# Optimization experiments

Hardware: AMD Instinct MI355X
Metric: run time of the kernel (lower is better)

The kernel has to match this reference:

```python
import jax, jax.numpy as jnp
import numpy as np

EMBED_DIM = 1024
NUM_HEADS = 16
HEAD_DIM = EMBED_DIM // NUM_HEADS
MAX_SEQ_LEN = 2048
ROPE_BASE = 10000.0


def _rope_tables(head_dim, max_seq_len, base):
    # inv_freq: (head_dim/2,)
    inv_freq = 1.0 / base ** (jnp.arange(0, head_dim, 2, dtype=jnp.float32) / head_dim)
    positions = jnp.arange(max_seq_len, dtype=jnp.float32)
    angles = positions[:, None] * inv_freq[None, :]  # (S, head_dim/2)
    # Original repeat_interleaves then slices [0::2], which recovers per-pair angles.
    return jnp.cos(angles), jnp.sin(angles)


def _apply_rope(x, cos, sin):
    # x: (B, H, S, D); cos/sin: (S, D/2)
    x_even = x[..., 0::2]
    x_odd = x[..., 1::2]
    c = cos[None, None, :, :]
    s = sin[None, None, :, :]
    x_even_rot = x_even * c - x_odd * s
    x_odd_rot = x_even * s + x_odd * c
    # interleave back: stack pairs on last dim and flatten
    x_rot = jnp.stack([x_even_rot, x_odd_rot], axis=-1)
    return x_rot.reshape(x.shape)


def setup_inputs() -> dict:
    key = jax.random.key(0)
    k1, k2, k3, k4 = jax.random.split(key, 4)
    B, S, E = 2, 2048, EMBED_DIM
    x = jax.random.normal(k1, (B, S, E), dtype=jnp.float32)
    bound_in = np.sqrt(6.0 / (3 * E + E)).astype(np.float32)
    in_proj_weight = jax.random.uniform(k2, (3 * E, E), minval=-bound_in, maxval=bound_in, dtype=jnp.float32)
    in_proj_bias = jnp.zeros((3 * E,), dtype=jnp.float32)
    bound_out = np.sqrt(6.0 / (E + E)).astype(np.float32)
    out_proj_weight = jax.random.uniform(k3, (E, E), minval=-bound_out, maxval=bound_out, dtype=jnp.float32)
    out_proj_bias = jnp.zeros((E,), dtype=jnp.float32)
    return {
        "query": x,
        "key": x,
        "value": x,
        "in_proj_weight": in_proj_weight,
        "in_proj_bias": in_proj_bias,
        "out_proj_weight": out_proj_weight,
        "out_proj_bias": out_proj_bias,
    }


def reference(query, key, value, in_proj_weight, in_proj_bias, out_proj_weight, out_proj_bias):
    B, S, E = query.shape
    H, D = NUM_HEADS, HEAD_DIM
    cos, sin = _rope_tables(D, MAX_SEQ_LEN, ROPE_BASE)
    cos, sin = cos[:S], sin[:S]

    # fused QKV projection (note: original applies in_proj to `query` only — self-attention)
    qkv = query @ in_proj_weight.T + in_proj_bias  # (B, S, 3E)
    q, k, v = jnp.split(qkv, 3, axis=-1)
    q = q.reshape(B, S, H, D).transpose(0, 2, 1, 3)  # (B, H, S, D)
    k = k.reshape(B, S, H, D).transpose(0, 2, 1, 3)
    v = v.reshape(B, S, H, D).transpose(0, 2, 1, 3)

    q = _apply_rope(q, cos, sin)
    k = _apply_rope(k, cos, sin)

    scale = 1.0 / np.sqrt(D).astype(np.float32)
    scores = jnp.einsum("bhqd,bhkd->bhqk", q, k) * scale
    attn = jax.nn.softmax(scores, axis=-1)
    out = jnp.einsum("bhqk,bhkd->bhqd", attn, v)  # (B, H, S, D)
    out = out.transpose(0, 2, 1, 3).reshape(B, S, E)
    return out @ out_proj_weight.T + out_proj_bias
```

## Files before the change

### kernel.cpp

```cpp
#include <hip/hip_runtime.h>
#include <hip/hip_bf16.h>
#include <cstdint>
#include <cstddef>

typedef __bf16 bf16;
typedef bf16 bf16x2 __attribute__((ext_vector_type(2)));
typedef bf16 bf16x4 __attribute__((ext_vector_type(4)));
typedef bf16 bf16x8 __attribute__((ext_vector_type(8)));
typedef float f32x4 __attribute__((ext_vector_type(4)));
typedef float f32x16 __attribute__((ext_vector_type(16)));

#define SEQ 2048
#define EMB 1024
#define NH 16
#define HD 64
#define BSZ 2
#define MROWS (BSZ*SEQ)

__device__ __forceinline__ void gload_lds16(const void* g, void* lds) {
  __builtin_amdgcn_global_load_lds((__attribute__((address_space(1))) void*)g,
                                   (__attribute__((address_space(3))) void*)lds,
                                   16, 0, 0);
}

__global__ void prep_kernel(const float* __restrict__ s0, bf16* __restrict__ d0, int n0_4,
                            const float* __restrict__ s1, bf16* __restrict__ d1, int n1_4,
                            const float* __restrict__ s2, bf16* __restrict__ d2, int n2_4,
                            float* __restrict__ cosT, float* __restrict__ sinT) {
  int j = blockIdx.x * blockDim.x + threadIdx.x;
  const float* s; bf16* d;
  if (j < n0_4) { s = s0; d = d0; }
  else {
    int j1 = j - n0_4;
    if (j1 < n1_4) { s = s1; d = d1; j = j1; }
    else {
      int j2 = j1 - n1_4;
      if (j2 < n2_4) { s = s2; d = d2; j = j2; }
      else {
        int idx = j2 - n2_4;
        if (idx >= SEQ * 32) return;
        int ss = idx >> 5, jj = idx & 31;
        float ex = (2.0f * (float)jj) / 64.0f;
        float inv = 1.0f / powf(10000.0f, ex);
        float ang = (float)ss * inv;
        cosT[idx] = cosf(ang);
        sinT[idx] = sinf(ang);
        return;
      }
    }
  }
  const float4 v = reinterpret_cast<const float4*>(s)[j];
  bf16x4 o;
  o[0] = (bf16)v.x; o[1] = (bf16)v.y; o[2] = (bf16)v.z; o[3] = (bf16)v.w;
  reinterpret_cast<bf16x4*>(d)[j] = o;
}

template<int EPI, int BM>
__launch_bounds__(256)
__global__ void gemm_bt(const bf16* __restrict__ A, const bf16* __restrict__ B,
                        const float* __restrict__ bias,
                        float* __restrict__ Cf,
                        bf16* __restrict__ qb, bf16* __restrict__ kb, bf16* __restrict__ vt,
                        const float* __restrict__ cosT, const float* __restrict__ sinT,
                        int Ndim, int Kdim) {
  constexpr int MREP = BM / 32;
  __shared__ __align__(16) bf16 Alds[2][BM * 32];
  __shared__ __align__(16) bf16 Blds[2][128 * 32];
  const int tid = threadIdx.x;
  const int wave = tid >> 6, lane = tid & 63;
  const int wr = wave >> 1, wc = wave & 1;
  const int bm = blockIdx.x * BM, bn = blockIdx.y * 128;

  f32x4 acc[MREP][4] = {};

  const int srow = lane >> 2;
  const int scol = (((lane & 3) ^ ((lane >> 3) & 3)) * 8);
  const int rchunk = (((lane >> 4) ^ ((lane >> 1) & 3)) * 8);

  for (int kt = 0; kt < Kdim; kt += 64) {
#pragma unroll
    for (int hf = 0; hf < 2; hf++) {
      char* aldsb = (char*)Alds[hf];
      char* bldsb = (char*)Blds[hf];
      const int kc = kt + hf * 32;
#pragma unroll
      for (int c = 0; c < BM / 64; c++)
        gload_lds16(A + (size_t)(bm + (wave + 4 * c) * 16 + srow) * Kdim + kc + scol,
                    aldsb + wave * 1024 + c * 4096);
      gload_lds16(B + (size_t)(bn + wave * 16 + srow) * Kdim + kc + scol, bldsb + wave * 1024);
      gload_lds16(B + (size_t)(bn + (wave + 4) * 16 + srow) * Kdim + kc + scol, bldsb + wave * 1024 + 4096);
    }
    __syncthreads();
#pragma unroll
    for (int hf = 0; hf < 2; hf++) {
      bf16x8 af[MREP], bfr[4];
#pragma unroll
      for (int m = 0; m < MREP; m++)
        af[m] = *reinterpret_cast<const bf16x8*>(Alds[hf] + (wr * (BM / 2) + m * 16 + (lane & 15)) * 32 + rchunk);
#pragma unroll
      for (int n = 0; n < 4; n++)
        bfr[n] = *reinterpret_cast<const bf16x8*>(Blds[hf] + (wc * 64 + n * 16 + (lane & 15)) * 32 + rchunk);
#pragma unroll
      for (int m = 0; m < MREP; m++)
#pragma unroll
        for (int n = 0; n < 4; n++)
          acc[m][n] = __builtin_amdgcn_mfma_f32_16x16x32_bf16(af[m], bfr[n], acc[m][n], 0, 0, 0);
    }
    __syncthreads();
  }

  if (EPI == 1 && bn >= 2 * EMB) {
#pragma unroll
    for (int m = 0; m < MREP; m++) {
#pragma unroll
      for (int n = 0; n < 4; n++) {
        const int col = bn + wc * 64 + n * 16 + (lane & 15);
        const int rem = col & 1023;
        const int h = rem >> 6, d = rem & 63;
        const int row0 = bm + wr * (BM / 2) + m * 16 + (lane >> 4) * 4;
        const int b = row0 >> 11, s0 = row0 & (SEQ - 1);
        const int g = (s0 >> 2) & 3;
        const int s0p = (s0 & ~15) | ((((g & 1) << 1) | (g >> 1)) << 2);
        const float bs = bias[col];
        bf16x4 o;
#pragma unroll
        for (int r = 0; r < 4; r++) o[r] = (bf16)(acc[m][n][r] + bs);
        *reinterpret_cast<bf16x4*>(vt + (((size_t)(b * NH + h) * HD) + d) * SEQ + s0p) = o;
      }
    }
  } else {
#pragma unroll
    for (int m = 0; m < MREP; m++) {
#pragma unroll
      for (int n = 0; n < 4; n++) {
#pragma unroll
        for (int r = 0; r < 4; r++) {
          const int row = bm + wr * (BM / 2) + m * 16 + (lane >> 4) * 4 + r;
          const int col = bn + wc * 64 + n * 16 + (lane & 15);
          const float v = acc[m][n][r] + bias[col];
          if (EPI == 0) {
            Cf[(size_t)row * Ndim + col] = v;
          } else {
            const int b = row >> 11, s = row & (SEQ - 1);
            const int which = col >> 10, rem = col & 1023;
            const int h = rem >> 6, d = rem & 63;
            const float vp = __shfl_xor(v, 1, 64);
            const int jj = d >> 1;
            const float c = cosT[(s << 5) + jj], sn = sinT[(s << 5) + jj];
            float vr = (d & 1) ? (vp * sn + v * c) : (v * c - vp * sn);
            if (which == 0) {
              vr *= 0.18033688f;
              qb[(((size_t)(b * NH + h) * SEQ) + s) * HD + d] = (bf16)vr;
            } else {
              kb[(((size_t)(b * NH + h) * SEQ) + s) * HD + d] = (bf16)vr;
            }
          }
        }
      }
    }
  }
}

__device__ __forceinline__ unsigned pk2(float a, float b) {
  bf16x2 t; t[0] = (bf16)a; t[1] = (bf16)b;
  unsigned u; __builtin_memcpy(&u, &t, 4); return u;
}

#if __has_builtin(__builtin_amdgcn_exp2f)
#define FEXP2(x) __builtin_amdgcn_exp2f(x)
#else
#define FEXP2(x) exp2f(x)
#endif

#define SSHIFT (-17.3123405f)

#define KPITCH 144

#define STAGE_LOAD(KV0) do { \
  kr0 = *(const int4*)(Kb + (size_t)((KV0) + (gtid >> 3)) * HD + (gtid & 7) * 8); \
  kr1 = *(const int4*)(Kb + (size_t)((KV0) + 32 + (gtid >> 3)) * HD + (gtid & 7) * 8); \
  vr0 = *(const int4*)(Vb + (size_t)(gtid >> 3) * SEQ + (KV0) + (gtid & 7) * 8); \
  vr1 = *(const int4*)(Vb + (size_t)(32 + (gtid >> 3)) * SEQ + (KV0) + (gtid & 7) * 8); \
} while (0)

#define STAGE_WRITE(BUF) do { \
  *(int4*)(Klds[grp][BUF] + (gtid >> 3) * KPITCH + (gtid & 7) * 16) = kr0; \
  *(int4*)(Klds[grp][BUF] + ((gtid >> 3) + 32) * KPITCH + (gtid & 7) * 16) = kr1; \
  *(int4*)(Vlds[grp][BUF] + (gtid >> 3) * KPITCH + (gtid & 7) * 16) = vr0; \
  *(int4*)(Vlds[grp][BUF] + ((gtid >> 3) + 32) * KPITCH + (gtid & 7) * 16) = vr1; \
} while (0)

#define COMPUTE_TILE64(BUFI) do { \
  const char* kbp = Klds[grp][BUFI]; const char* vbp = Vlds[grp][BUFI]; \
  bf16x8 KF[2][4], VF[2][4]; \
  _Pragma("unroll") \
  for (int hh = 0; hh < 2; hh++) \
    _Pragma("unroll") \
    for (int dk = 0; dk < 4; dk++) \
      KF[hh][dk] = *reinterpret_cast<const bf16x8*>(kbp + (hh * 32 + ql) * KPITCH + dk * 32 + hi * 16); \
  _Pragma("unroll") \
  for (int hh = 0; hh < 2; hh++) \
    _Pragma("unroll") \
    for (int i = 0; i < 4; i++) \
      VF[hh][i] = *reinterpret_cast<const bf16x8*>(vbp + ((i >> 1) * 32 + ql) * KPITCH + hh * 64 + (i & 1) * 32 + hi * 16); \
   \
  f32x16 s0 = __builtin_amdgcn_mfma_f32_32x32x16_bf16(KF[0][0], qf[0], sinit, 0, 0, 0); \
  f32x16 s1 = __builtin_amdgcn_mfma_f32_32x32x16_bf16(KF[1][0], qf[0], sinit, 0, 0, 0); \
  __builtin_amdgcn_s_setprio(1); \
  _Pragma("unroll") \
  for (int dk = 1; dk < 4; dk++) { \
    s0 = __builtin_amdgcn_mfma_f32_32x32x16_bf16(KF[0][dk], qf[dk], s0, 0, 0, 0); \
    s1 = __builtin_amdgcn_mfma_f32_32x32x16_bf16(KF[1][dk], qf[dk], s1, 0, 0, 0); \
  } \
  __builtin_amdgcn_s_setprio(0); \
  float p0[16], p1[16]; \
  _Pragma("unroll") \
  for (int r = 0; r < 16; r++) { p0[r] = FEXP2(s0[r]); p1[r] = FEXP2(s1[r]); } \
  _Pragma("unroll") \
  for (int r = 0; r < 16; r++) psum[r] += p0[r] + p1[r]; \
   \
  bf16x8 pf[2][2]; \
  { \
    unsigned w00[4] = { pk2(p0[0], p0[1]),  pk2(p0[2], p0[3]),   pk2(p0[4], p0[5]),   pk2(p0[6], p0[7]) }; \
    unsigned w01[4] = { pk2(p0[8], p0[9]),  pk2(p0[10], p0[11]), pk2(p0[12], p0[13]), pk2(p0[14], p0[15]) }; \
    unsigned w10[4] = { pk2(p1[0], p1[1]),  pk2(p1[2], p1[3]),   pk2(p1[4], p1[5]),   pk2(p1[6], p1[7]) }; \
    unsigned w11[4] = { pk2(p1[8], p1[9]),  pk2(p1[10], p1[11]), pk2(p1[12], p1[13]), pk2(p1[14], p1[15]) }; \
    __builtin_memcpy(&pf[0][0], w00, 16); \
    __builtin_memcpy(&pf[0][1], w01, 16); \
    __builtin_memcpy(&pf[1][0], w10, 16); \
    __builtin_memcpy(&pf[1][1], w11, 16); \
  } \
  __builtin_amdgcn_s_setprio(1); \
  _Pragma("unroll") \
  for (int hh = 0; hh < 2; hh++) { \
    oacc0 = __builtin_amdgcn_mfma_f32_32x32x16_bf16(VF[hh][0], pf[hh][0], oacc0, 0, 0, 0); \
    oacc0 = __builtin_amdgcn_mfma_f32_32x32x16_bf16(VF[hh][1], pf[hh][1], oacc0, 0, 0, 0); \
    oacc1 = __builtin_amdgcn_mfma_f32_32x32x16_bf16(VF[hh][2], pf[hh][0], oacc1, 0, 0, 0); \
    oacc1 = __builtin_amdgcn_mfma_f32_32x32x16_bf16(VF[hh][3], pf[hh][1], oacc1, 0, 0, 0); \
  } \
  __builtin_amdgcn_s_setprio(0); \
} while (0)

__launch_bounds__(512)
__global__ void attn_kernel(const bf16* __restrict__ qb, const bf16* __restrict__ kb,
                            const bf16* __restrict__ vt, bf16* __restrict__ ob) {
  const int bid = (blockIdx.x & 7) * 64 + (blockIdx.x >> 3);
  const int qblk = bid & 15;
  const int bh = bid >> 4;
  const int b = bh >> 4, h = bh & 15;
  const int tid = threadIdx.x;
  const int wave = tid >> 6;
  const int grp = wave >> 2;
  const int wsub = wave & 3;
  const int gtid = tid & 255;
  const int lane = tid & 63;
  const int q0 = qblk * 128 + wsub * 32;
  const int ql = lane & 31, hi = lane >> 5;

  __shared__ __align__(16) char Klds[2][2][64 * KPITCH];
  __shared__ __align__(16) char Vlds[2][2][64 * KPITCH];

  const bf16* Qb = qb + (size_t)bh * SEQ * HD;
  const bf16* Kb = kb + (size_t)bh * SEQ * HD + (size_t)grp * 1024 * HD;
  const bf16* Vb = vt + (size_t)bh * HD * SEQ + grp * 1024;

  bf16x8 qf[4];
#pragma unroll
  for (int dk = 0; dk < 4; dk++)
    qf[dk] = *reinterpret_cast<const bf16x8*>(Qb + (size_t)(q0 + ql) * HD + dk * 16 + hi * 8);

  f32x16 sinit;
#pragma unroll
  for (int r = 0; r < 16; r++) sinit[r] = SSHIFT;

  f32x16 oacc0 = {}, oacc1 = {};
  float psum[16];
#pragma unroll
  for (int r = 0; r < 16; r++) psum[r] = 0.f;

  int4 kr0, kr1, vr0, vr1;
  STAGE_LOAD(0);
  STAGE_WRITE(0);
  __syncthreads();

  for (int t = 0; t < 16; ++t) {
    const int cur = t & 1;
    if (t < 15) STAGE_LOAD((t + 1) * 64);
    COMPUTE_TILE64(cur);
    if (t < 15) STAGE_WRITE(cur ^ 1);
    __syncthreads();
  }

#pragma unroll
  for (int r = 0; r < 8; r++) psum[r] += psum[r + 8];
#pragma unroll
  for (int r = 0; r < 4; r++) psum[r] += psum[r + 4];
  float lrun = (psum[0] + psum[1]) + (psum[2] + psum[3]);
  lrun += __shfl_xor(lrun, 32, 64);

  float* cb = (float*)(&Klds[0][0][0]);
  float* myb = cb + (wsub * 64 + lane) * 36;
  if (grp == 1) {
#pragma unroll
    for (int q = 0; q < 4; q++) {
      *reinterpret_cast<f32x4*>(myb + 4 * q) =
          f32x4{oacc0[4 * q], oacc0[4 * q + 1], oacc0[4 * q + 2], oacc0[4 * q + 3]};
      *reinterpret_cast<f32x4*>(myb + 16 + 4 * q) =
          f32x4{oacc1[4 * q], oacc1[4 * q + 1], oacc1[4 * q + 2], oacc1[4 * q + 3]};
    }
    myb[32] = lrun;
  }
  __syncthreads();
  if (grp == 0) {
    const float inv = 1.0f / (lrun + myb[32]);
    const size_t orow = ((size_t)b * SEQ + q0 + ql) * EMB + h * HD;
#pragma unroll
    for (int q = 0; q < 4; q++) {
      const f32x4 m0 = *reinterpret_cast<const f32x4*>(myb + 4 * q);
      const f32x4 m1 = *reinterpret_cast<const f32x4*>(myb + 16 + 4 * q);
      bf16x4 o0, o1;
#pragma unroll
      for (int j = 0; j < 4; j++) {
        o0[j] = (bf16)((oacc0[4 * q + j] + m0[j]) * inv);
        o1[j] = (bf16)((oacc1[4 * q + j] + m1[j]) * inv);
      }
      const int d = 8 * q + 4 * hi;
      *reinterpret_cast<bf16x4*>(ob + orow + d)      = o0;
      *reinterpret_cast<bf16x4*>(ob + orow + 32 + d) = o1;
    }
  }
}

extern "C" void kernel_launch(void* const* d_in, const int* in_sizes, int n_in,
                              void* d_out, int out_size, void* d_ws, size_t ws_size,
                              hipStream_t stream) {
  const float* x    = (const float*)d_in[0];
  const float* Win  = (const float*)d_in[3];
  const float* bin  = (const float*)d_in[4];
  const float* Wout = (const float*)d_in[5];
  const float* bout = (const float*)d_in[6];
  float* out = (float*)d_out;

  char* p = (char*)d_ws;
  bf16* xb  = (bf16*)p; p += (size_t)MROWS * EMB * 2;
  bf16* wb  = (bf16*)p; p += (size_t)3 * EMB * EMB * 2;
  bf16* wob = (bf16*)p; p += (size_t)EMB * EMB * 2;
  bf16* qb  = (bf16*)p; p += (size_t)MROWS * EMB * 2;
  bf16* kb  = (bf16*)p; p += (size_t)MROWS * EMB * 2;
  bf16* vt  = (bf16*)p; p += (size_t)MROWS * EMB * 2;
  bf16* ob  = (bf16*)p; p += (size_t)MROWS * EMB * 2;
  float* cosT = (float*)p; p += (size_t)SEQ * 32 * 4;
  float* sinT = (float*)p; p += (size_t)SEQ * 32 * 4;

  const int n0 = MROWS * EMB / 4, n1 = 3 * EMB * EMB / 4, n2 = EMB * EMB / 4;
  const int ntot = n0 + n1 + n2 + SEQ * 32;
  prep_kernel<<<(ntot + 255) / 256, 256, 0, stream>>>(x, xb, n0, Win, wb, n1, Wout, wob, n2, cosT, sinT);

  gemm_bt<1, 64><<<dim3(MROWS / 64, 3 * EMB / 128), 256, 0, stream>>>(
      xb, wb, bin, nullptr, qb, kb, vt, cosT, sinT, 3 * EMB, EMB);
  attn_kernel<<<BSZ * NH * (SEQ / 128), 512, 0, stream>>>(qb, kb, vt, ob);
  gemm_bt<0, 64><<<dim3(MROWS / 64, EMB / 128), 256, 0, stream>>>(
      ob, wob, bout, out, nullptr, nullptr, nullptr, nullptr, nullptr, EMB, EMB);
}
```

Measured before the change: 118.0 us.

## Stage K/V tiles via direct global-to-LDS loads with XOR-swizzled layout

```diff
diff --git a/kernel.cpp b/kernel.cpp
--- a/kernel.cpp
+++ b/kernel.cpp
@@ -121,11 +121,12 @@
         const int b = row0 >> 11, s0 = row0 & (SEQ - 1);
         const int g = (s0 >> 2) & 3;
         const int s0p = (s0 & ~15) | ((((g & 1) << 1) | (g >> 1)) << 2);
+        const int s0q = s0p ^ ((d & 7) << 3);
         const float bs = bias[col];
         bf16x4 o;
 #pragma unroll
         for (int r = 0; r < 4; r++) o[r] = (bf16)(acc[m][n][r] + bs);
-        *reinterpret_cast<bf16x4*>(vt + (((size_t)(b * NH + h) * HD) + d) * SEQ + s0p) = o;
+        *reinterpret_cast<bf16x4*>(vt + (((size_t)(b * NH + h) * HD) + d) * SEQ + s0q) = o;
       }
     }
   } else {
@@ -152,7 +153,7 @@
               vr *= 0.18033688f;
               qb[(((size_t)(b * NH + h) * SEQ) + s) * HD + d] = (bf16)vr;
             } else {
-              kb[(((size_t)(b * NH + h) * SEQ) + s) * HD + d] = (bf16)vr;
+              kb[(((size_t)(b * NH + h) * SEQ) + s) * HD + (d ^ ((s & 7) << 3))] = (bf16)vr;
             }
           }
         }
@@ -174,35 +175,29 @@
 
 #define SSHIFT (-17.3123405f)
 
-#define KPITCH 144
-
-#define STAGE_LOAD(KV0) do { \
-  kr0 = *(const int4*)(Kb + (size_t)((KV0) + (gtid >> 3)) * HD + (gtid & 7) * 8); \
-  kr1 = *(const int4*)(Kb + (size_t)((KV0) + 32 + (gtid >> 3)) * HD + (gtid & 7) * 8); \
-  vr0 = *(const int4*)(Vb + (size_t)(gtid >> 3) * SEQ + (KV0) + (gtid & 7) * 8); \
-  vr1 = *(const int4*)(Vb + (size_t)(32 + (gtid >> 3)) * SEQ + (KV0) + (gtid & 7) * 8); \
+#define STAGE_G(BUF, KV0) do { \
+  char* kd_ = LDSM + (grp * 2 + (BUF)) * 8192 + wsub * 1024; \
+  char* vd_ = LDSM + 32768 + (grp * 2 + (BUF)) * 8192 + wsub * 1024; \
+  gload_lds16(Kb + (size_t)((KV0) + srowA) * HD + schunk, kd_); \
+  gload_lds16(Kb + (size_t)((KV0) + 32 + srowA) * HD + schunk, kd_ + 4096); \
+  gload_lds16(Vb + (size_t)srowA * SEQ + (KV0) + schunk, vd_); \
+  gload_lds16(Vb + (size_t)(32 + srowA) * SEQ + (KV0) + schunk, vd_ + 4096); \
 } while (0)
 
-#define STAGE_WRITE(BUF) do { \
-  *(int4*)(Klds[grp][BUF] + (gtid >> 3) * KPITCH + (gtid & 7) * 16) = kr0; \
-  *(int4*)(Klds[grp][BUF] + ((gtid >> 3) + 32) * KPITCH + (gtid & 7) * 16) = kr1; \
-  *(int4*)(Vlds[grp][BUF] + (gtid >> 3) * KPITCH + (gtid & 7) * 16) = vr0; \
-  *(int4*)(Vlds[grp][BUF] + ((gtid >> 3) + 32) * KPITCH + (gtid & 7) * 16) = vr1; \
-} while (0)
-
 #define COMPUTE_TILE64(BUFI) do { \
-  const char* kbp = Klds[grp][BUFI]; const char* vbp = Vlds[grp][BUFI]; \
+  const char* kbp = LDSM + (grp * 2 + (BUFI)) * 8192; \
+  const char* vbp = LDSM + 32768 + (grp * 2 + (BUFI)) * 8192; \
   bf16x8 KF[2][4], VF[2][4]; \
   _Pragma("unroll") \
   for (int hh = 0; hh < 2; hh++) \
     _Pragma("unroll") \
     for (int dk = 0; dk < 4; dk++) \
-      KF[hh][dk] = *reinterpret_cast<const bf16x8*>(kbp + (hh * 32 + ql) * KPITCH + dk * 32 + hi * 16); \
+      KF[hh][dk] = *reinterpret_cast<const bf16x8*>(kbp + (hh * 32 + ql) * 128 + (((dk * 2 + hi) ^ (ql & 7)) * 16)); \
   _Pragma("unroll") \
   for (int hh = 0; hh < 2; hh++) \
     _Pragma("unroll") \
     for (int i = 0; i < 4; i++) \
-      VF[hh][i] = *reinterpret_cast<const bf16x8*>(vbp + ((i >> 1) * 32 + ql) * KPITCH + hh * 64 + (i & 1) * 32 + hi * 16); \
+      VF[hh][i] = *reinterpret_cast<const bf16x8*>(vbp + ((i >> 1) * 32 + ql) * 128 + (((hh * 4 + (i & 1) * 2 + hi) ^ (ql & 7)) * 16)); \
    \
   f32x16 s0 = __builtin_amdgcn_mfma_f32_32x32x16_bf16(KF[0][0], qf[0], sinit, 0, 0, 0); \
   f32x16 s1 = __builtin_amdgcn_mfma_f32_32x32x16_bf16(KF[1][0], qf[0], sinit, 0, 0, 0); \
@@ -257,13 +252,15 @@
   const int q0 = qblk * 128 + wsub * 32;
   const int ql = lane & 31, hi = lane >> 5;
 
-  __shared__ __align__(16) char Klds[2][2][64 * KPITCH];
-  __shared__ __align__(16) char Vlds[2][2][64 * KPITCH];
+  __shared__ __align__(16) char LDSM[65536];
 
   const bf16* Qb = qb + (size_t)bh * SEQ * HD;
   const bf16* Kb = kb + (size_t)bh * SEQ * HD + (size_t)grp * 1024 * HD;
   const bf16* Vb = vt + (size_t)bh * HD * SEQ + grp * 1024;
 
+  const int srowA = gtid >> 3;
+  const int schunk = (gtid & 7) * 8;
+
   bf16x8 qf[4];
 #pragma unroll
   for (int dk = 0; dk < 4; dk++)
@@ -278,16 +275,13 @@
 #pragma unroll
   for (int r = 0; r < 16; r++) psum[r] = 0.f;
 
-  int4 kr0, kr1, vr0, vr1;
-  STAGE_LOAD(0);
-  STAGE_WRITE(0);
+  STAGE_G(0, 0);
   __syncthreads();
 
   for (int t = 0; t < 16; ++t) {
     const int cur = t & 1;
-    if (t < 15) STAGE_LOAD((t + 1) * 64);
+    if (t < 15) STAGE_G(cur ^ 1, (t + 1) * 64);
     COMPUTE_TILE64(cur);
-    if (t < 15) STAGE_WRITE(cur ^ 1);
     __syncthreads();
   }
 
@@ -298,7 +292,7 @@
   float lrun = (psum[0] + psum[1]) + (psum[2] + psum[3]);
   lrun += __shfl_xor(lrun, 32, 64);
 
-  float* cb = (float*)(&Klds[0][0][0]);
+  float* cb = (float*)(&LDSM[0]);
   float* myb = cb + (wsub * 64 + lane) * 36;
   if (grp == 1) {
 #pragma unroll
```

Measured after the change: 121.7 us. 3.2% more time.
